# Kernel optimization log

Measured on AMD Instinct MI355X. Metric: run time of the kernel, lower is better.

The kernel has to match this reference:

```python
import jax, jax.numpy as jnp
import numpy as np

# Neuron / sim constants (match init_kwargs)
TAU = 10.0
THR = 1.0
WIDTH_GRAD = 1.0   # surrogate width (beta)
SCALE_GRAD = 1.0   # surrogate scale
ALPHA = float(np.exp(-1.0 / TAU))  # sinabs LIF decay, dt=1


@jax.custom_vjp
def spike(v):
    # SingleSpike: binary spike when membrane crosses threshold
    return (v >= THR).astype(v.dtype)

def _spike_fwd(v):
    return (v >= THR).astype(v.dtype), v

def _spike_bwd(v, g):
    # SingleExponential surrogate: scale * exp(-|v - thr| / width)
    surr = SCALE_GRAD * jnp.exp(-jnp.abs(v - THR) / WIDTH_GRAD)
    return (g * surr,)

spike.defvjp(_spike_fwd, _spike_bwd)


def lif_scan(weighted):
    """weighted: [B, N, T] synaptic current -> spikes [B, N, T]."""
    i_seq = jnp.moveaxis(weighted, -1, 0)  # [T, B, N]

    def step(v, i_t):
        # sinabs LIF (norm_input=True): decay + normalized input
        v = ALPHA * v + (1.0 - ALPHA) * i_t
        s = spike(v)
        v = v - s * THR  # MembraneSubtract reset
        return v, s

    v0 = jnp.zeros_like(i_seq[0])
    _, spikes_seq = jax.lax.scan(step, v0, i_seq)
    return jnp.moveaxis(spikes_seq, 0, -1)  # [B, N, T]


def setup_inputs() -> dict:
    key = jax.random.key(0)
    kx, kw = jax.random.split(key)
    B, C, H, W_, T = 32768, 2, 4, 4, 100
    x = jax.random.normal(kx, (B, C, H, W_, T), dtype=jnp.float32)
    W = jax.random.normal(kw, (1, C * H * W_), dtype=jnp.float32) * (1.0 / np.sqrt(C * H * W_))
    return {"x": x, "W": W}


def reference(x, W):
    B, T = x.shape[0], x.shape[-1]
    xf = x.reshape(B, -1, T)                  # [B, 32, T]
    weighted = jnp.einsum("of,bft->bot", W, xf)  # dense projection -> [B, 1, T]
    return lif_scan(weighted)                 # spikes [B, 1, T]
```

## Files before the change

kernel.cpp:

```cpp
#include <hip/hip_runtime.h>


#define NB     32
#define BLOCK  256
#define TT     100
#define FF     32
#define T4     (TT/4)
#define ROWPAD 128

__global__ __launch_bounds__(BLOCK) void exodus_lif_kernel(
        const float* __restrict__ x,
        const float* __restrict__ Wg,
        float* __restrict__ out)
{
    __shared__ __align__(16) float wbuf[NB * ROWPAD];

    const int  tid = threadIdx.x;
    const long b0  = (long)blockIdx.x * NB;

    const int NITEM = NB * T4;
    for (int item = tid; item < NITEM; item += BLOCK) {
        const int bl = item / T4;
        const int t4 = item % T4;
        const float4* xp =
            reinterpret_cast<const float4*>(x + (b0 + bl) * (long)(FF * TT) + t4 * 4);
        float4 acc = make_float4(0.f, 0.f, 0.f, 0.f);
#pragma unroll
        for (int f = 0; f < FF; ++f) {
            const float4 xv = xp[f * T4];
            const float  w  = Wg[f];
            acc.x += w * xv.x;
            acc.y += w * xv.y;
            acc.z += w * xv.z;
            acc.w += w * xv.w;
        }
        const int t4s = t4 ^ (bl & 7);
        *reinterpret_cast<float4*>(&wbuf[bl * ROWPAD + t4s * 4]) = acc;
    }
    __syncthreads();

    if (tid < NB) {
        const float A  = 0.90483741803595952f;
        const float OM = 0.09516258196404048f;
        const int   bl = tid;
        float v = 0.f;
#pragma unroll
        for (int t4 = 0; t4 < T4; ++t4) {
            const int t4s = t4 ^ (bl & 7);
            float4 w = *reinterpret_cast<float4*>(&wbuf[bl * ROWPAD + t4s * 4]);
            float* we = &w.x;
#pragma unroll
            for (int k = 0; k < 4; ++k) {
                v = A * v + OM * we[k];
                const float s = (v >= 1.0f) ? 1.0f : 0.0f;
                v -= s;
                we[k] = s;
            }
            *reinterpret_cast<float4*>(&wbuf[bl * ROWPAD + t4s * 4]) = w;
        }
    }
    __syncthreads();

    for (int item = tid; item < NITEM; item += BLOCK) {
        const int bl  = item / T4;
        const int t4  = item % T4;
        const int t4s = t4 ^ (bl & 7);
        const float4 s = *reinterpret_cast<const float4*>(&wbuf[bl * ROWPAD + t4s * 4]);
        *reinterpret_cast<float4*>(out + (b0 + bl) * (long)TT + t4 * 4) = s;
    }
}

extern "C" void kernel_launch(void* const* d_in, const int* in_sizes, int n_in,
                              void* d_out, int out_size, void* d_ws, size_t ws_size,
                              hipStream_t stream) {
    const float* x  = (const float*)d_in[0];
    const float* Wg = (const float*)d_in[1];
    float* out      = (float*)d_out;

    const int B    = in_sizes[0] / (FF * TT);
    const int grid = B / NB;

    exodus_lif_kernel<<<grid, BLOCK, 0, stream>>>(x, Wg, out);
}
```

Measured before the change: 83.62 us.

## Give each wavefront its own rows and replace block barriers with wave-local waits

Splits the block's 32 rows so each of the 4 wavefronts projects, scans and stores its own 8 rows, replacing __syncthreads with per-wave LDS waitcnts. This removes block-wide barrier stalls during the serial LIF scan so other waves can keep loading. The projection sum is split into two accumulator chains for more ILP. It relies on intra-wave lockstep LDS ordering instead of explicit barriers.

```diff
diff --git a/kernel.cpp b/kernel.cpp
--- a/kernel.cpp
+++ b/kernel.cpp
@@ -1,11 +1,13 @@
 #include <hip/hip_runtime.h>
 
 
-#define NB     32
+#define RPW    8
+#define WAVES  4
+#define NB     (RPW * WAVES)
 #define BLOCK  256
 #define TT     100
 #define FF     32
-#define T4     (TT/4)
+#define T4     (TT / 4)
 #define ROWPAD 128
 
 __global__ __launch_bounds__(BLOCK) void exodus_lif_kernel(
@@ -15,39 +17,47 @@
 {
     __shared__ __align__(16) float wbuf[NB * ROWPAD];
 
-    const int  tid = threadIdx.x;
-    const long b0  = (long)blockIdx.x * NB;
+    const int  tid  = threadIdx.x;
+    const int  wv   = tid >> 6;
+    const int  lane = tid & 63;
+    const long b0   = (long)blockIdx.x * NB + wv * RPW;
+    float* const wlds = &wbuf[(wv * RPW) * ROWPAD];
 
-    const int NITEM = NB * T4;
-    for (int item = tid; item < NITEM; item += BLOCK) {
-        const int bl = item / T4;
-        const int t4 = item % T4;
+    const int NIT = RPW * T4;
+    for (int i = lane; i < NIT; i += 64) {
+        const int rl = i / T4;
+        const int t4 = i % T4;
         const float4* xp =
-            reinterpret_cast<const float4*>(x + (b0 + bl) * (long)(FF * TT) + t4 * 4);
-        float4 acc = make_float4(0.f, 0.f, 0.f, 0.f);
+            reinterpret_cast<const float4*>(x + (b0 + rl) * (long)(FF * TT) + t4 * 4);
+        float4 a0 = make_float4(0.f, 0.f, 0.f, 0.f);
+        float4 a1 = make_float4(0.f, 0.f, 0.f, 0.f);
 #pragma unroll
-        for (int f = 0; f < FF; ++f) {
+        for (int f = 0; f < 16; ++f) {
             const float4 xv = xp[f * T4];
             const float  w  = Wg[f];
-            acc.x += w * xv.x;
-            acc.y += w * xv.y;
-            acc.z += w * xv.z;
-            acc.w += w * xv.w;
+            a0.x += w * xv.x; a0.y += w * xv.y; a0.z += w * xv.z; a0.w += w * xv.w;
         }
-        const int t4s = t4 ^ (bl & 7);
-        *reinterpret_cast<float4*>(&wbuf[bl * ROWPAD + t4s * 4]) = acc;
+#pragma unroll
+        for (int f = 16; f < 32; ++f) {
+            const float4 xv = xp[f * T4];
+            const float  w  = Wg[f];
+            a1.x += w * xv.x; a1.y += w * xv.y; a1.z += w * xv.z; a1.w += w * xv.w;
+        }
+        a0.x += a1.x; a0.y += a1.y; a0.z += a1.z; a0.w += a1.w;
+        const int t4s = t4 ^ (rl & 7);
+        *reinterpret_cast<float4*>(&wlds[rl * ROWPAD + t4s * 4]) = a0;
     }
-    __syncthreads();
+    asm volatile("s_waitcnt lgkmcnt(0)" ::: "memory");
 
-    if (tid < NB) {
+    if (lane < RPW) {
         const float A  = 0.90483741803595952f;
         const float OM = 0.09516258196404048f;
-        const int   bl = tid;
+        const int   rl = lane;
         float v = 0.f;
 #pragma unroll
         for (int t4 = 0; t4 < T4; ++t4) {
-            const int t4s = t4 ^ (bl & 7);
-            float4 w = *reinterpret_cast<float4*>(&wbuf[bl * ROWPAD + t4s * 4]);
+            const int t4s = t4 ^ (rl & 7);
+            float4 w = *reinterpret_cast<float4*>(&wlds[rl * ROWPAD + t4s * 4]);
             float* we = &w.x;
 #pragma unroll
             for (int k = 0; k < 4; ++k) {
@@ -56,17 +66,17 @@
                 v -= s;
                 we[k] = s;
             }
-            *reinterpret_cast<float4*>(&wbuf[bl * ROWPAD + t4s * 4]) = w;
+            *reinterpret_cast<float4*>(&wlds[rl * ROWPAD + t4s * 4]) = w;
         }
     }
-    __syncthreads();
+    asm volatile("s_waitcnt lgkmcnt(0)" ::: "memory");
 
-    for (int item = tid; item < NITEM; item += BLOCK) {
-        const int bl  = item / T4;
-        const int t4  = item % T4;
-        const int t4s = t4 ^ (bl & 7);
-        const float4 s = *reinterpret_cast<const float4*>(&wbuf[bl * ROWPAD + t4s * 4]);
-        *reinterpret_cast<float4*>(out + (b0 + bl) * (long)TT + t4 * 4) = s;
+    for (int i = lane; i < NIT; i += 64) {
+        const int rl  = i / T4;
+        const int t4  = i % T4;
+        const int t4s = t4 ^ (rl & 7);
+        const float4 s = *reinterpret_cast<const float4*>(&wlds[rl * ROWPAD + t4s * 4]);
+        *reinterpret_cast<float4*>(out + (b0 + rl) * (long)TT + t4 * 4) = s;
     }
 }
 
```

Result: slower. 86.06 us (+2.9%).
